# Performance work log

Hardware: AMD Instinct MI355X
Metric: run time of the kernel (lower is better)

The kernel has to match this reference:

```python
import jax, jax.numpy as jnp
import numpy as np
from functools import partial

# Block hyperparams (match init_kwargs)
B, C, N, H = 16, 512, 1024, 8
HID = 4 * C
TAU, THRESH, SG_SCALE = 2.0, 1.0, 5.0
ATTN_SCALE = 0.25
BN_EPS = 1e-5

# LIF spiking neuron (single-step, stateless): membrane v = x / tau, hard threshold
# forward; sigmoid surrogate gradient (scale=5.0) in backward.
@partial(jax.custom_vjp, nondiff_argnums=(1,))
def spike(u, scale):
    return (u >= 0.0).astype(u.dtype)

def _spike_fwd(u, scale):
    return spike(u, scale), u

def _spike_bwd(scale, u, g):
    s = jax.nn.sigmoid(scale * u)
    return (g * scale * s * (1.0 - s),)

spike.defvjp(_spike_fwd, _spike_bwd)

def lif(x):
    return spike(x / TAU - THRESH, SG_SCALE)

def conv1x1(x, w, b=None):
    # x: [B,C,N], w: [O,C] -> [B,O,N]
    y = jnp.einsum('oc,bcn->bon', w, x)
    return y if b is None else y + b[None, :, None]

def bn(x, g, b):
    # BatchNorm1d, training-mode batch stats over (batch, length), biased var
    m = jnp.mean(x, axis=(0, 2), keepdims=True)
    v = jnp.var(x, axis=(0, 2), keepdims=True)
    return (x - m) * jax.lax.rsqrt(v + BN_EPS) * g[None, :, None] + b[None, :, None]


def setup_inputs() -> dict:
    key = jax.random.key(0)
    ks = jax.random.split(key, 8)
    w = lambda k, o, i: jax.random.normal(k, (o, i), dtype=jnp.float32) * 0.02
    inp = {
        'x': jax.random.normal(ks[0], (B, C, N), dtype=jnp.float32),
        'q_w': w(ks[1], C, C), 'q_g': jnp.ones((C,), jnp.float32), 'q_b': jnp.zeros((C,), jnp.float32),
        'k_w': w(ks[2], C, C), 'k_g': jnp.ones((C,), jnp.float32), 'k_b': jnp.zeros((C,), jnp.float32),
        'v_w': w(ks[3], C, C), 'v_g': jnp.ones((C,), jnp.float32), 'v_b': jnp.zeros((C,), jnp.float32),
        'proj_w': w(ks[4], C, C), 'proj_bias': jnp.zeros((C,), jnp.float32),
        'proj_g': jnp.ones((C,), jnp.float32), 'proj_b': jnp.zeros((C,), jnp.float32),
        'fc1_w': w(ks[5], HID, C), 'fc1_bias': jnp.zeros((HID,), jnp.float32),
        'fc1_g': jnp.ones((HID,), jnp.float32), 'fc1_b': jnp.zeros((HID,), jnp.float32),
        'fc2_w': w(ks[6], C, HID), 'fc2_bias': jnp.zeros((C,), jnp.float32),
        'fc2_g': jnp.ones((C,), jnp.float32), 'fc2_b': jnp.zeros((C,), jnp.float32),
    }
    return inp


def reference(x, q_w, q_g, q_b, k_w, k_g, k_b, v_w, v_g, v_b,
              proj_w, proj_bias, proj_g, proj_b,
              fc1_w, fc1_bias, fc1_g, fc1_b, fc2_w, fc2_bias, fc2_g, fc2_b):
    Bb, Cc, Nn = x.shape
    D = Cc // H

    def heads(t):  # [B,C,N] -> [B,H,N,D]
        return t.transpose(0, 2, 1).reshape(Bb, Nn, H, D).transpose(0, 2, 1, 3)

    # spiking attention (no softmax): (Q K^T) V * 0.25
    q = heads(lif(bn(conv1x1(x, q_w), q_g, q_b)))
    k = heads(lif(bn(conv1x1(x, k_w), k_g, k_b)))
    v = heads(lif(bn(conv1x1(x, v_w), v_g, v_b)))
    scores = jnp.einsum('bhnd,bhmd->bhnm', q, k)            # [B,H,N,N]
    attn = jnp.einsum('bhnm,bhmd->bhnd', scores, v) * ATTN_SCALE
    a = attn.transpose(0, 1, 3, 2).reshape(Bb, Cc, Nn)       # [B,C,N]
    a = lif(a)
    a = lif(bn(conv1x1(a, proj_w, proj_bias), proj_g, proj_b))
    x = x + a                                                # residual 1

    # conv1x1-BN-LIF MLP
    h = lif(bn(conv1x1(x, fc1_w, fc1_bias), fc1_g, fc1_b))
    h = lif(bn(conv1x1(h, fc2_w, fc2_bias), fc2_g, fc2_b))
    return x + h                                             # residual 2
```

## Files before the change

kernel.cpp:

```cpp
#include <hip/hip_runtime.h>
#include <stdint.h>

#pragma clang fp contract(off)

#define BATCH 16
#define CCH   512
#define NLEN  1024
#define NH    8
#define DH    64

__device__ float pw128(const float* __restrict__ x) {
    float r0=x[0],r1=x[1],r2=x[2],r3=x[3],r4=x[4],r5=x[5],r6=x[6],r7=x[7];
    for (int i = 8; i < 128; i += 8) {
        r0 += x[i+0]; r1 += x[i+1]; r2 += x[i+2]; r3 += x[i+3];
        r4 += x[i+4]; r5 += x[i+5]; r6 += x[i+6]; r7 += x[i+7];
    }
    return ((r0+r1)+(r2+r3))+((r4+r5)+(r6+r7));
}
__device__ float pw128_sqdev(const float* __restrict__ x, float m) {
    float r0,r1,r2,r3,r4,r5,r6,r7;
    {
        float d;
        d = x[0]-m; r0 = d*d;  d = x[1]-m; r1 = d*d;
        d = x[2]-m; r2 = d*d;  d = x[3]-m; r3 = d*d;
        d = x[4]-m; r4 = d*d;  d = x[5]-m; r5 = d*d;
        d = x[6]-m; r6 = d*d;  d = x[7]-m; r7 = d*d;
    }
    for (int i = 8; i < 128; i += 8) {
        float d;
        d = x[i+0]-m; r0 += d*d;  d = x[i+1]-m; r1 += d*d;
        d = x[i+2]-m; r2 += d*d;  d = x[i+3]-m; r3 += d*d;
        d = x[i+4]-m; r4 += d*d;  d = x[i+5]-m; r5 += d*d;
        d = x[i+6]-m; r6 += d*d;  d = x[i+7]-m; r7 += d*d;
    }
    return ((r0+r1)+(r2+r3))+((r4+r5)+(r6+r7));
}

__global__ __launch_bounds__(64) void bn_stats_np_k(const float* __restrict__ Y, int O,
                                                    float2* __restrict__ st)
{
    const int o = blockIdx.x;
    const int t = threadIdx.x;
    const int bi = t >> 2, q = t & 3;
    __shared__ float part[64];
    __shared__ float msh;
    const float* p = Y + ((size_t)bi * O + o) * NLEN + q * 256;
    {
        float s0 = pw128(p), s1 = pw128(p + 128);
        part[t] = s0 + s1;
    }
    __syncthreads();
    if (t == 0) {
        float s = 0.0f;
        for (int b = 0; b < 16; ++b) {
            const float* pp = &part[b * 4];
            float v = (pp[0] + pp[1]) + (pp[2] + pp[3]);
            s = (b == 0) ? v : (s + v);
        }
        msh = s / 16384.0f;
    }
    __syncthreads();
    const float m = msh;
    {
        float s0 = pw128_sqdev(p, m), s1 = pw128_sqdev(p + 128, m);
        part[t] = s0 + s1;
    }
    __syncthreads();
    if (t == 0) {
        float s = 0.0f;
        for (int b = 0; b < 16; ++b) {
            const float* pp = &part[b * 4];
            float v = (pp[0] + pp[1]) + (pp[2] + pp[3]);
            s = (b == 0) ? v : (s + v);
        }
        float var = s / 16384.0f;
        float ve  = var + 1e-5f;
        float sq  = (float)sqrt((double)ve);
        float r   = (float)(1.0 / (double)sq);
        st[o] = make_float2(m, r);
    }
}

__device__ inline bool spike_f32(float y, float2 s, float g, float b) {
    float t1 = y - s.x;
    float t2 = t1 * s.y;
    float t3 = t2 * g;
    float t4 = t3 + b;
    float u  = t4 / 2.0f - 1.0f;
    return u >= 0.0f;
}

template<int MODE>
__global__ __launch_bounds__(256) void gemm_k(
    const float* __restrict__ Wt, const float* __restrict__ Xf, const uint8_t* __restrict__ Xs8,
    const float* __restrict__ bias, float* __restrict__ Y,
    int O, int Cin, int N, int ldW)
{
    __shared__ float Xs[2][16][132];
    const int b = blockIdx.z;
    const size_t xbase = (size_t)b * Cin * N;
    float* Yb = Y + (size_t)b * O * N;
    const int o0 = blockIdx.y * 128;
    const int n0 = blockIdx.x * 128;
    const int t  = threadIdx.x;
    const int tx = t & 15;
    const int ty = t >> 4;

    const int xk = t >> 4;
    const int xc = (t & 15) << 3;

    float acc[8][8];
#pragma unroll
    for (int i = 0; i < 8; ++i)
#pragma unroll
        for (int j = 0; j < 8; ++j) acc[i][j] = 0.0f;

    float xr[8];

    auto loadGX = [&](int k0) {
        size_t off = xbase + (size_t)(k0 + xk) * N + n0 + xc;
        float4 v0 = *reinterpret_cast<const float4*>(Xf + off);
        float4 v1 = *reinterpret_cast<const float4*>(Xf + off + 4);
        if (MODE == 0) {
            xr[0]=v0.x; xr[1]=v0.y; xr[2]=v0.z; xr[3]=v0.w;
            xr[4]=v1.x; xr[5]=v1.y; xr[6]=v1.z; xr[7]=v1.w;
        } else {
            uchar4 u0 = *reinterpret_cast<const uchar4*>(Xs8 + off);
            uchar4 u1 = *reinterpret_cast<const uchar4*>(Xs8 + off + 4);
            xr[0]=v0.x+(float)u0.x; xr[1]=v0.y+(float)u0.y;
            xr[2]=v0.z+(float)u0.z; xr[3]=v0.w+(float)u0.w;
            xr[4]=v1.x+(float)u1.x; xr[5]=v1.y+(float)u1.y;
            xr[6]=v1.z+(float)u1.z; xr[7]=v1.w+(float)u1.w;
        }
    };
    auto stageX = [&](int buf) {
        *reinterpret_cast<float4*>(&Xs[buf][xk][xc])     = make_float4(xr[0],xr[1],xr[2],xr[3]);
        *reinterpret_cast<float4*>(&Xs[buf][xk][xc + 4]) = make_float4(xr[4],xr[5],xr[6],xr[7]);
    };

    const float* wbase = Wt + o0 + ty * 4;

    loadGX(0);
    stageX(0);
    __syncthreads();
    int cur = 0;
    for (int k0 = 0;;) {
        const int kn = k0 + 16;
        const bool more = kn < Cin;
        if (more) loadGX(kn);
#pragma unroll
        for (int kq = 0; kq < 4; ++kq) {
            float4 a0[4], a1[4];
            const float* wrow = wbase + (size_t)(k0 + kq * 4) * ldW;
#pragma unroll
            for (int u = 0; u < 4; ++u) {
                a0[u] = *reinterpret_cast<const float4*>(wrow + (size_t)u * ldW);
                a1[u] = *reinterpret_cast<const float4*>(wrow + (size_t)u * ldW + 64);
            }
#pragma unroll
            for (int u = 0; u < 4; ++u) {
                const int kk = kq * 4 + u;
                float4 b0 = *reinterpret_cast<const float4*>(&Xs[cur][kk][tx * 4]);
                float4 b1 = *reinterpret_cast<const float4*>(&Xs[cur][kk][64 + tx * 4]);
                float av[8] = {a0[u].x,a0[u].y,a0[u].z,a0[u].w,a1[u].x,a1[u].y,a1[u].z,a1[u].w};
                float bv[8] = {b0.x,b0.y,b0.z,b0.w,b1.x,b1.y,b1.z,b1.w};
#pragma unroll
                for (int i = 0; i < 8; ++i)
#pragma unroll
                    for (int j = 0; j < 8; ++j)
                        acc[i][j] = fmaf(av[i], bv[j], acc[i][j]);
            }
        }
        if (!more) break;
        stageX(cur ^ 1);
        __syncthreads();
        cur ^= 1;
        k0 = kn;
    }
#pragma unroll
    for (int half = 0; half < 2; ++half)
#pragma unroll
        for (int i = 0; i < 4; ++i) {
            const int r = half * 4 + i;
            const int o = o0 + half * 64 + ty * 4 + i;
            const float bb = bias ? bias[o] : 0.0f;
            float* yp = Yb + (size_t)o * N + n0;
            float4 r0, r1;
            r0.x = acc[r][0] + bb; r0.y = acc[r][1] + bb;
            r0.z = acc[r][2] + bb; r0.w = acc[r][3] + bb;
            r1.x = acc[r][4] + bb; r1.y = acc[r][5] + bb;
            r1.z = acc[r][6] + bb; r1.w = acc[r][7] + bb;
            *reinterpret_cast<float4*>(yp + tx * 4)      = r0;
            *reinterpret_cast<float4*>(yp + 64 + tx * 4) = r1;
        }
}

__global__ __launch_bounds__(256) void wt_k(const float* __restrict__ W, float* __restrict__ Wt,
                                            int O, int Cin, int o_off, int Otot)
{
    __shared__ float tile[32][33];
    const int k0 = blockIdx.x * 32, o0 = blockIdx.y * 32;
    const int tx = threadIdx.x & 31, ty = threadIdx.x >> 5;
#pragma unroll
    for (int j = 0; j < 4; ++j)
        tile[ty + 8*j][tx] = W[(size_t)(o0 + ty + 8*j) * Cin + k0 + tx];
    __syncthreads();
#pragma unroll
    for (int j = 0; j < 4; ++j)
        Wt[(size_t)(k0 + ty + 8*j) * Otot + o_off + o0 + tx] = tile[tx][ty + 8*j];
}

__global__ __launch_bounds__(256) void col_bits_k(const uint8_t* __restrict__ S,
                                                  unsigned long long* __restrict__ bits, int Cin)
{
    const int n0 = blockIdx.x * 64, kw = blockIdx.y, b = blockIdx.z;
    __shared__ uint8_t tile[64][64];
    const int t = threadIdx.x;
    const int r = t >> 2, cg = (t & 3) * 16;
    const uint8_t* src = S + ((size_t)b * Cin + kw * 64 + r) * NLEN + n0 + cg;
    *reinterpret_cast<uint4*>(&tile[r][cg]) = *reinterpret_cast<const uint4*>(src);
    __syncthreads();
    if (t < 64) {
        unsigned long long m = 0;
#pragma unroll
        for (int rr = 0; rr < 64; ++rr)
            m |= ((unsigned long long)(tile[rr][t] != 0)) << rr;
        bits[((size_t)b * NLEN + n0 + t) * (Cin >> 6) + kw] = m;
    }
}

__global__ __launch_bounds__(256) void sparse_gemm_k(
    const float* __restrict__ Wt, const unsigned long long* __restrict__ bits,
    const float* __restrict__ bias, float* __restrict__ Y, int Cin)
{
    const int wid  = (blockIdx.x << 2) + (threadIdx.x >> 6);
    const int lane = threadIdx.x & 63;
    const int b = wid >> 10, n = wid & 1023;
    const int W64 = Cin >> 6;
    float acc[8];
#pragma unroll
    for (int i = 0; i < 8; ++i) acc[i] = 0.0f;
    const unsigned long long* bp = bits + ((size_t)b * NLEN + n) * W64;
    for (int w = 0; w < W64; ++w) {
        unsigned long long m = bp[w];
        while (m) {
            const int bit = __builtin_ctzll(m);
            m &= m - 1;
            const int k = (w << 6) + bit;
            const float* wr = Wt + ((size_t)k << 9) + lane * 8;
            float4 w0 = *reinterpret_cast<const float4*>(wr);
            float4 w1 = *reinterpret_cast<const float4*>(wr + 4);
            acc[0] += w0.x; acc[1] += w0.y; acc[2] += w0.z; acc[3] += w0.w;
            acc[4] += w1.x; acc[5] += w1.y; acc[6] += w1.z; acc[7] += w1.w;
        }
    }
    const float* bq = bias + lane * 8;
    float4 b0 = *reinterpret_cast<const float4*>(bq);
    float4 b1 = *reinterpret_cast<const float4*>(bq + 4);
    float bi[8] = {b0.x, b0.y, b0.z, b0.w, b1.x, b1.y, b1.z, b1.w};
    float* yp = Y + ((size_t)b * 512 + lane * 8) * NLEN + n;
#pragma unroll
    for (int i = 0; i < 8; ++i)
        yp[(size_t)i * NLEN] = acc[i] + bi[i];
}

__global__ __launch_bounds__(256) void spike_pack_qkv_k(
    const float* __restrict__ Y, const float2* __restrict__ st,
    const float* __restrict__ gq, const float* __restrict__ gk, const float* __restrict__ gv,
    const float* __restrict__ bq, const float* __restrict__ bk, const float* __restrict__ bv,
    uint8_t* __restrict__ oq, uint8_t* __restrict__ ok, uint8_t* __restrict__ ov)
{
    const int nt = blockIdx.x, hs = blockIdx.y, b = blockIdx.z;
    const int tensor = hs >> 3, h = hs & 7;
    const float* g  = (tensor == 0) ? gq : (tensor == 1) ? gk : gv;
    const float* be = (tensor == 0) ? bq : (tensor == 1) ? bk : bv;
    uint8_t* outp   = (tensor == 0) ? oq : (tensor == 1) ? ok : ov;
    __shared__ uint8_t tile[64][68];
    const int t = threadIdx.x;
    {
        const int i = t & 63, dq = t >> 6;
#pragma unroll
        for (int p = 0; p < 16; ++p) {
            int d  = dq * 16 + p;
            int cf = hs * 64 + d;
            int cl = h * 64 + d;
            float y = Y[((size_t)b * 1536 + cf) * NLEN + nt * 64 + i];
            tile[d][i] = spike_f32(y, st[cf], g[cl], be[cl]) ? 1 : 0;
        }
    }
    __syncthreads();
    {
        const int d = t & 63, iq = t >> 6;
#pragma unroll
        for (int p = 0; p < 16; ++p) {
            int i = iq * 16 + p;
            outp[((size_t)(b * NH + h) * NLEN + nt * 64 + i) * DH + d] = tile[d][i];
        }
    }
}

__global__ __launch_bounds__(256) void ktv_part_k(const uint8_t* __restrict__ Kb,
                                                  const uint8_t* __restrict__ Vb,
                                                  float* __restrict__ Mp)
{
    const int bh = blockIdx.x, ch = blockIdx.y;
    const uint8_t* kp = Kb + (size_t)bh * NLEN * DH;
    const uint8_t* vp = Vb + (size_t)bh * NLEN * DH;
    __shared__ float ks[64][68];
    __shared__ float vs[64][68];
    const int t = threadIdx.x;
    const int d2 = t & 63, g4 = t >> 6;
    float acc[16];
#pragma unroll
    for (int j = 0; j < 16; ++j) acc[j] = 0.f;

    for (int nc = ch * 128; nc < ch * 128 + 128; nc += 64) {
#pragma unroll
        for (int p = 0; p < 16; ++p) {
            int idx = t + p * 256;
            int r = idx >> 6, d = idx & 63;
            ks[r][d] = (float)kp[(size_t)(nc + r) * DH + d];
            vs[r][d] = (float)vp[(size_t)(nc + r) * DH + d];
        }
        __syncthreads();
        for (int n = 0; n < 64; ++n) {
            float vv = vs[n][d2];
#pragma unroll
            for (int j = 0; j < 16; ++j)
                acc[j] += ks[n][g4 * 16 + j] * vv;
        }
        __syncthreads();
    }
#pragma unroll
    for (int j = 0; j < 16; ++j)
        Mp[((size_t)ch * 128 + bh) * 4096 + (size_t)(g4 * 16 + j) * 64 + d2] = acc[j];
}

__global__ __launch_bounds__(256) void ktv_reduce_k(const float* __restrict__ Mp,
                                                    float* __restrict__ M)
{
    const int bh = blockIdx.x;
    const int t = threadIdx.x;
#pragma unroll
    for (int j = 0; j < 16; j += 4) {
        const int idx = t * 16 + j;
        float4 s = *reinterpret_cast<const float4*>(&Mp[(size_t)bh * 4096 + idx]);
#pragma unroll
        for (int c = 1; c < 8; ++c) {
            float4 v = *reinterpret_cast<const float4*>(&Mp[((size_t)c * 128 + bh) * 4096 + idx]);
            s.x += v.x; s.y += v.y; s.z += v.z; s.w += v.w;
        }
        *reinterpret_cast<float4*>(&M[(size_t)bh * 4096 + idx]) = s;
    }
}

__global__ __launch_bounds__(256) void attn_spike_k(const uint8_t* __restrict__ Qb, const float* __restrict__ M,
                                                    uint8_t* __restrict__ A)
{
    const int nt = blockIdx.x, h = blockIdx.y, b = blockIdx.z;
    const int bh = b * NH + h;
    __shared__ float Ms[64][68];
    __shared__ float qs[64][65];
    const int t = threadIdx.x;
#pragma unroll
    for (int p = 0; p < 16; ++p) {
        int idx = t + p * 256;
        int r = idx >> 6, c = idx & 63;
        Ms[r][c] = M[(size_t)bh * 4096 + idx];
        qs[c][r] = (float)Qb[((size_t)bh * NLEN + nt * 64 + r) * DH + c];
    }
    __syncthreads();
    const int n = t & 63, dg = t >> 6;
    float acc[16];
#pragma unroll
    for (int j = 0; j < 16; ++j) acc[j] = 0.f;
    for (int d1 = 0; d1 < 64; ++d1) {
        float qv = qs[d1][n];
#pragma unroll
        for (int j = 0; j < 16; ++j)
            acc[j] += qv * Ms[d1][dg * 16 + j];
    }
#pragma unroll
    for (int j = 0; j < 16; ++j) {
        int d = dg * 16 + j;
        A[((size_t)b * CCH + h * 64 + d) * NLEN + nt * 64 + n] = (acc[j] >= 8.0f) ? 1 : 0;
    }
}

__global__ __launch_bounds__(256) void spike_store_k(
    const float* __restrict__ Y, const float2* __restrict__ st,
    const float* __restrict__ g, const float* __restrict__ bet,
    uint8_t* __restrict__ H, int Oc, int o_off, int Otot)
{
    size_t i4 = (size_t)blockIdx.x * 256 + threadIdx.x;
    size_t total = (size_t)BATCH * Oc * (NLEN / 4);
    if (i4 >= total) return;
    int n4 = (int)(i4 & 255);
    int o  = (int)((i4 >> 8) % Oc);
    int b  = (int)(i4 / ((size_t)256 * Oc));
    float4 y = reinterpret_cast<const float4*>(Y)[i4];
    float2 s = st[o];
    float gg = g[o], bb = bet[o];
    uchar4 r;
    r.x = spike_f32(y.x, s, gg, bb) ? 1 : 0;
    r.y = spike_f32(y.y, s, gg, bb) ? 1 : 0;
    r.z = spike_f32(y.z, s, gg, bb) ? 1 : 0;
    r.w = spike_f32(y.w, s, gg, bb) ? 1 : 0;
    *reinterpret_cast<uchar4*>(H + ((size_t)(b * Otot + o_off + o)) * NLEN + n4 * 4) = r;
}

__global__ __launch_bounds__(256) void final_k(
    const float* __restrict__ Y, const float2* __restrict__ st,
    const float* __restrict__ g, const float* __restrict__ bet,
    const float* __restrict__ x, const uint8_t* __restrict__ ares,
    float* __restrict__ Out)
{
    size_t i4 = (size_t)blockIdx.x * 256 + threadIdx.x;
    size_t total = (size_t)BATCH * CCH * (NLEN / 4);
    if (i4 >= total) return;
    int o = (int)((i4 >> 8) % CCH);
    float4 y  = reinterpret_cast<const float4*>(Y)[i4];
    float4 xv = reinterpret_cast<const float4*>(x)[i4];
    uchar4 av = reinterpret_cast<const uchar4*>(ares)[i4];
    float2 s = st[o];
    float gg = g[o], bb = bet[o];
    float4 r;
    {
        float x1;
        x1 = xv.x + (float)av.x; r.x = x1 + (spike_f32(y.x, s, gg, bb) ? 1.0f : 0.0f);
        x1 = xv.y + (float)av.y; r.y = x1 + (spike_f32(y.y, s, gg, bb) ? 1.0f : 0.0f);
        x1 = xv.z + (float)av.z; r.z = x1 + (spike_f32(y.z, s, gg, bb) ? 1.0f : 0.0f);
        x1 = xv.w + (float)av.w; r.w = x1 + (spike_f32(y.w, s, gg, bb) ? 1.0f : 0.0f);
    }
    reinterpret_cast<float4*>(Out)[i4] = r;
}

extern "C" void kernel_launch(void* const* d_in, const int* in_sizes, int n_in,
                              void* d_out, int out_size, void* d_ws, size_t ws_size,
                              hipStream_t stream)
{
    const float* x         = (const float*)d_in[0];
    const float* q_w       = (const float*)d_in[1];
    const float* q_g       = (const float*)d_in[2];
    const float* q_b       = (const float*)d_in[3];
    const float* k_w       = (const float*)d_in[4];
    const float* k_g       = (const float*)d_in[5];
    const float* k_b       = (const float*)d_in[6];
    const float* v_w       = (const float*)d_in[7];
    const float* v_g       = (const float*)d_in[8];
    const float* v_b       = (const float*)d_in[9];
    const float* proj_w    = (const float*)d_in[10];
    const float* proj_bias = (const float*)d_in[11];
    const float* proj_g    = (const float*)d_in[12];
    const float* proj_b    = (const float*)d_in[13];
    const float* fc1_w     = (const float*)d_in[14];
    const float* fc1_bias  = (const float*)d_in[15];
    const float* fc1_g     = (const float*)d_in[16];
    const float* fc1_b     = (const float*)d_in[17];
    const float* fc2_w     = (const float*)d_in[18];
    const float* fc2_bias  = (const float*)d_in[19];
    const float* fc2_g     = (const float*)d_in[20];
    const float* fc2_b     = (const float*)d_in[21];
    float* out = (float*)d_out;

    char* ws = (char*)d_ws;
    const size_t MiB = 1ull << 20;
    if (ws_size < 124 * MiB) return;

    float*    Yq    = (float*)(ws);
    float*    Af    = (float*)(ws);
    uint8_t*  ab    = (uint8_t*)(ws);
    float*    Mpart = (float*)(ws + 16 * MiB);
    uint8_t*  ares  = (uint8_t*)(ws + 64 * MiB);
    uint8_t*  hb    = (uint8_t*)(ws + 72 * MiB);
    uint8_t*  qb    = (uint8_t*)(ws + 96 * MiB);
    uint8_t*  kb    = (uint8_t*)(ws + 104 * MiB);
    uint8_t*  vb    = (uint8_t*)(ws + 112 * MiB);
    float*    Wt    = (float*)(ws + 104 * MiB);
    unsigned long long* bits = (unsigned long long*)(ws + 108 * MiB);
    float*    Wtq   = (float*)(ws + 120 * MiB);
    float*    Mbuf  = (float*)(ws + 120 * MiB);
    float2*   stats = (float2*)(ws + 123 * MiB);

    dim3 thr256(256);

    wt_k<<<dim3(16, 16), thr256, 0, stream>>>(q_w, Wtq, 512, 512,    0, 1536);
    wt_k<<<dim3(16, 16), thr256, 0, stream>>>(k_w, Wtq, 512, 512,  512, 1536);
    wt_k<<<dim3(16, 16), thr256, 0, stream>>>(v_w, Wtq, 512, 512, 1024, 1536);
    gemm_k<0><<<dim3(8, 12, 16), thr256, 0, stream>>>(Wtq, x, nullptr, nullptr, Yq,
                                                      1536, 512, 1024, 1536);
    bn_stats_np_k<<<dim3(1536), dim3(64), 0, stream>>>(Yq, 1536, stats);
    spike_pack_qkv_k<<<dim3(16, 24, 16), thr256, 0, stream>>>(Yq, stats, q_g, k_g, v_g,
                                                              q_b, k_b, v_b, qb, kb, vb);

    ktv_part_k<<<dim3(128, 8), thr256, 0, stream>>>(kb, vb, Mpart);
    ktv_reduce_k<<<dim3(128), thr256, 0, stream>>>(Mpart, Mbuf);
    attn_spike_k<<<dim3(16, 8, 16), thr256, 0, stream>>>(qb, Mbuf, ab);

    wt_k<<<dim3(16, 16), thr256, 0, stream>>>(proj_w, Wt, 512, 512, 0, 512);
    col_bits_k<<<dim3(16, 8, 16), thr256, 0, stream>>>(ab, bits, 512);
    sparse_gemm_k<<<dim3(4096), thr256, 0, stream>>>(Wt, bits, proj_bias, Af, 512);
    bn_stats_np_k<<<dim3(512), dim3(64), 0, stream>>>(Af, 512, stats);
    spike_store_k<<<dim3(8192), thr256, 0, stream>>>(Af, stats, proj_g, proj_b, ares, 512, 0, 512);

    wt_k<<<dim3(16, 64), thr256, 0, stream>>>(fc1_w, Wt, 2048, 512, 0, 2048);
    for (int ch = 0; ch < 2; ++ch) {
        gemm_k<2><<<dim3(8, 8, 16), thr256, 0, stream>>>(Wt + ch * 1024, x, ares,
                                                         fc1_bias + ch * 1024, Af,
                                                         1024, 512, 1024, 2048);
        bn_stats_np_k<<<dim3(1024), dim3(64), 0, stream>>>(Af, 1024, stats);
        spike_store_k<<<dim3(16384), thr256, 0, stream>>>(Af, stats, fc1_g + ch * 1024, fc1_b + ch * 1024,
                                                          hb, 1024, ch * 1024, 2048);
    }

    wt_k<<<dim3(64, 16), thr256, 0, stream>>>(fc2_w, Wt, 512, 2048, 0, 512);
    col_bits_k<<<dim3(16, 32, 16), thr256, 0, stream>>>(hb, bits, 2048);
    sparse_gemm_k<<<dim3(4096), thr256, 0, stream>>>(Wt, bits, fc2_bias, Af, 2048);
    bn_stats_np_k<<<dim3(512), dim3(64), 0, stream>>>(Af, 512, stats);
    final_k<<<dim3(8192), thr256, 0, stream>>>(Af, stats, fc2_g, fc2_b, x, ares, out);
}
```

Measured before the change: 1.631 ms.

## Remap GEMM thread tiles so each wave reads weights as uniform scalar loads

```diff
diff --git a/kernel.cpp b/kernel.cpp
--- a/kernel.cpp
+++ b/kernel.cpp
@@ -103,17 +103,15 @@
     const int o0 = blockIdx.y * 128;
     const int n0 = blockIdx.x * 128;
     const int t  = threadIdx.x;
-    const int tx = t & 15;
-    const int ty = t >> 4;
+    const int wid  = __builtin_amdgcn_readfirstlane(t >> 6);
+    const int lane = t & 63;
 
     const int xk = t >> 4;
     const int xc = (t & 15) << 3;
 
-    float acc[8][8];
-#pragma unroll
-    for (int i = 0; i < 8; ++i)
-#pragma unroll
-        for (int j = 0; j < 8; ++j) acc[i][j] = 0.0f;
+    float acc[32][2];
+#pragma unroll
+    for (int r = 0; r < 32; ++r) { acc[r][0] = 0.0f; acc[r][1] = 0.0f; }
 
     float xr[8];
 
@@ -138,7 +136,7 @@
         *reinterpret_cast<float4*>(&Xs[buf][xk][xc + 4]) = make_float4(xr[4],xr[5],xr[6],xr[7]);
     };
 
-    const float* wbase = Wt + o0 + ty * 4;
+    const float* wcol = Wt + o0 + wid * 32;
 
     loadGX(0);
     stageX(0);
@@ -149,26 +147,14 @@
         const bool more = kn < Cin;
         if (more) loadGX(kn);
 #pragma unroll
-        for (int kq = 0; kq < 4; ++kq) {
-            float4 a0[4], a1[4];
-            const float* wrow = wbase + (size_t)(k0 + kq * 4) * ldW;
-#pragma unroll
-            for (int u = 0; u < 4; ++u) {
-                a0[u] = *reinterpret_cast<const float4*>(wrow + (size_t)u * ldW);
-                a1[u] = *reinterpret_cast<const float4*>(wrow + (size_t)u * ldW + 64);
-            }
-#pragma unroll
-            for (int u = 0; u < 4; ++u) {
-                const int kk = kq * 4 + u;
-                float4 b0 = *reinterpret_cast<const float4*>(&Xs[cur][kk][tx * 4]);
-                float4 b1 = *reinterpret_cast<const float4*>(&Xs[cur][kk][64 + tx * 4]);
-                float av[8] = {a0[u].x,a0[u].y,a0[u].z,a0[u].w,a1[u].x,a1[u].y,a1[u].z,a1[u].w};
-                float bv[8] = {b0.x,b0.y,b0.z,b0.w,b1.x,b1.y,b1.z,b1.w};
-#pragma unroll
-                for (int i = 0; i < 8; ++i)
-#pragma unroll
-                    for (int j = 0; j < 8; ++j)
-                        acc[i][j] = fmaf(av[i], bv[j], acc[i][j]);
+        for (int kk = 0; kk < 16; ++kk) {
+            const float* ap = wcol + (size_t)(k0 + kk) * ldW;
+            float2 bv = *reinterpret_cast<const float2*>(&Xs[cur][kk][lane * 2]);
+#pragma unroll
+            for (int r = 0; r < 32; ++r) {
+                const float a = ap[r];
+                acc[r][0] = fmaf(a, bv.x, acc[r][0]);
+                acc[r][1] = fmaf(a, bv.y, acc[r][1]);
             }
         }
         if (!more) break;
@@ -178,21 +164,14 @@
         k0 = kn;
     }
 #pragma unroll
-    for (int half = 0; half < 2; ++half)
-#pragma unroll
-        for (int i = 0; i < 4; ++i) {
-            const int r = half * 4 + i;
-            const int o = o0 + half * 64 + ty * 4 + i;
-            const float bb = bias ? bias[o] : 0.0f;
-            float* yp = Yb + (size_t)o * N + n0;
-            float4 r0, r1;
-            r0.x = acc[r][0] + bb; r0.y = acc[r][1] + bb;
-            r0.z = acc[r][2] + bb; r0.w = acc[r][3] + bb;
-            r1.x = acc[r][4] + bb; r1.y = acc[r][5] + bb;
-            r1.z = acc[r][6] + bb; r1.w = acc[r][7] + bb;
-            *reinterpret_cast<float4*>(yp + tx * 4)      = r0;
-            *reinterpret_cast<float4*>(yp + 64 + tx * 4) = r1;
-        }
+    for (int r = 0; r < 32; ++r) {
+        const int o = o0 + wid * 32 + r;
+        const float bb = bias ? bias[o] : 0.0f;
+        float2 v;
+        v.x = acc[r][0] + bb;
+        v.y = acc[r][1] + bb;
+        *reinterpret_cast<float2*>(Yb + (size_t)o * N + n0 + lane * 2) = v;
+    }
 }
 
 __global__ __launch_bounds__(256) void wt_k(const float* __restrict__ W, float* __restrict__ Wt,
```

After: 2.137 ms. 31.0% more time.
